# Kernel tuning notes

Measured on AMD Instinct MI355X. Metric: run time of the kernel, lower is better.

## Reference

```python
import jax, jax.numpy as jnp
import numpy as np

N = 50000
E = 800000


def sage_conv(x, edge_index, W_l, b_l, W_r):
    """PyG SAGEConv with mean aggregation.

    out = lin_l(mean_{j in N(i)} x_j) + lin_r(x_i)
    lin_l has bias, lin_r (root weight) has no bias.
    """
    src, dst = edge_index[0], edge_index[1]
    n = x.shape[0]
    msg_sum = jax.ops.segment_sum(x[src], dst, num_segments=n)          # [N, F]
    cnt = jax.ops.segment_sum(jnp.ones((edge_index.shape[1],), x.dtype), dst,
                              num_segments=n)                           # [N]
    mean = msg_sum / jnp.maximum(cnt, 1.0)[:, None]
    return mean @ W_l + b_l + x @ W_r


def setup_inputs() -> dict:
    key = jax.random.key(0)
    ks = jax.random.split(key, 10)
    dims = [(128, 128), (128, 128), (128, 64)]
    inp = {
        "x": jax.random.normal(ks[0], (N, 128), dtype=jnp.float32),
        "edge_index": jax.random.randint(ks[1], (2, E), 0, N, dtype=jnp.int64),
    }
    for i, (fi, fo) in enumerate(dims):
        scale = 1.0 / np.sqrt(fi)
        inp[f"W_l{i}"] = jax.random.uniform(ks[2 + 3 * i - (3 * i) % 1], (fi, fo), jnp.float32, -scale, scale)
        inp[f"b_l{i}"] = jnp.zeros((fo,), jnp.float32)
        inp[f"W_r{i}"] = jax.random.uniform(jax.random.fold_in(ks[3], i), (fi, fo), jnp.float32, -scale, scale)
        inp[f"W_l{i}"] = jax.random.uniform(jax.random.fold_in(ks[2], i), (fi, fo), jnp.float32, -scale, scale)
    return inp


def reference(x, edge_index, W_l0, b_l0, W_r0, W_l1, b_l1, W_r1, W_l2, b_l2, W_r2):
    # Layer 1 + relu (dropout identity in eval mode)
    h = jax.nn.relu(sage_conv(x, edge_index, W_l0, b_l0, W_r0))
    # Layer 2 + relu
    h = jax.nn.relu(sage_conv(h, edge_index, W_l1, b_l1, W_r1))
    # Output layer (no activation)
    return sage_conv(h, edge_index, W_l2, b_l2, W_r2)
```

## Files before the change

### kernel.cpp

```cpp
#include <hip/hip_runtime.h>

static inline int ceil_div(int a, int b) { return (a + b - 1) / b; }

typedef __attribute__((ext_vector_type(8))) short short8;
typedef __attribute__((ext_vector_type(4))) float f32x4;

__device__ __forceinline__ ushort bf16_rne(float v) {
  uint u = __float_as_uint(v);
  return (ushort)((u + 0x7FFFu + ((u >> 16) & 1u)) >> 16);
}


__global__ void k_zero_int(int* __restrict__ p, int n) {
  int i = blockIdx.x * blockDim.x + threadIdx.x;
  if (i < n) p[i] = 0;
}

__global__ void k_count_rank(const int* __restrict__ dst, int* __restrict__ cnt,
                             int* __restrict__ rank, int e) {
  int i0 = (blockIdx.x * blockDim.x + threadIdx.x) * 4;
  if (i0 >= e) return;
  int d[4], r[4];
  if (i0 + 3 < e) {
    int4 dv = *(const int4*)(dst + i0);
    d[0] = dv.x; d[1] = dv.y; d[2] = dv.z; d[3] = dv.w;
  } else {
#pragma unroll
    for (int j = 0; j < 4; ++j) d[j] = (i0 + j < e) ? dst[i0 + j] : 0;
  }
#pragma unroll
  for (int j = 0; j < 4; ++j)
    if (i0 + j < e) r[j] = atomicAdd(&cnt[d[j]], 1);
  if (i0 + 3 < e) {
    *(int4*)(rank + i0) = make_int4(r[0], r[1], r[2], r[3]);
  } else {
#pragma unroll
    for (int j = 0; j < 4; ++j)
      if (i0 + j < e) rank[i0 + j] = r[j];
  }
}

#define SCAN_BS 256
#define SCAN_VPT 4
#define SCAN_CHUNK (SCAN_BS * SCAN_VPT)

__global__ __launch_bounds__(SCAN_BS) void k_blocksum(const int* __restrict__ cnt,
                                                      int* __restrict__ partial, int n) {
  __shared__ int s[SCAN_BS / 64];
  const int tid = threadIdx.x;
  const int base = blockIdx.x * SCAN_CHUNK;
  int sum = 0;
#pragma unroll
  for (int j = 0; j < SCAN_VPT; ++j) {
    int i = base + tid + j * SCAN_BS;
    if (i < n) sum += cnt[i];
  }
#pragma unroll
  for (int off = 32; off > 0; off >>= 1) sum += __shfl_down(sum, off, 64);
  if ((tid & 63) == 0) s[tid >> 6] = sum;
  __syncthreads();
  if (tid == 0) {
    int t = 0;
#pragma unroll
    for (int w = 0; w < SCAN_BS / 64; ++w) t += s[w];
    partial[blockIdx.x] = t;
  }
}

__global__ __launch_bounds__(256) void k_scan_partials(int* __restrict__ partial, int p,
                                                       int* __restrict__ row_ptr, int n_nodes) {
  __shared__ int s[256];
  const int tid = threadIdx.x;
  int carry = 0;
  for (int base = 0; base < p; base += 256) {
    int i = base + tid;
    int v = (i < p) ? partial[i] : 0;
    s[tid] = v;
    __syncthreads();
    for (int off = 1; off < 256; off <<= 1) {
      int t = (tid >= off) ? s[tid - off] : 0;
      __syncthreads();
      s[tid] += t;
      __syncthreads();
    }
    if (i < p) partial[i] = carry + s[tid] - v;
    int tot = s[255];
    __syncthreads();
    carry += tot;
  }
  if (tid == 0) row_ptr[n_nodes] = carry;
}

__global__ __launch_bounds__(SCAN_BS) void k_scatter(const int* __restrict__ cnt,
                                                     const int* __restrict__ partial,
                                                     int* __restrict__ row_ptr,
                                                     float* __restrict__ inv, int n) {
  __shared__ int s[SCAN_BS];
  const int tid = threadIdx.x;
  const int base = blockIdx.x * SCAN_CHUNK;
  const int i0 = base + tid * SCAN_VPT;
  int v[SCAN_VPT];
  int cv[SCAN_VPT];
  int sum = 0;
#pragma unroll
  for (int j = 0; j < SCAN_VPT; ++j) {
    int i = i0 + j;
    int c = (i < n) ? cnt[i] : 0;
    cv[j] = c;
    v[j] = sum;
    sum += c;
  }
  s[tid] = sum;
  __syncthreads();
  for (int off = 1; off < SCAN_BS; off <<= 1) {
    int t = (tid >= off) ? s[tid - off] : 0;
    __syncthreads();
    s[tid] += t;
    __syncthreads();
  }
  const int excl = partial[blockIdx.x] + s[tid] - sum;
#pragma unroll
  for (int j = 0; j < SCAN_VPT; ++j) {
    int i = i0 + j;
    if (i < n) {
      row_ptr[i] = excl + v[j];
      inv[i] = 1.0f / (float)(cv[j] > 1 ? cv[j] : 1);
    }
  }
}

__global__ void k_place(const int* __restrict__ src, const int* __restrict__ dst,
                        const int* __restrict__ rank, const int* __restrict__ row_ptr,
                        ushort* __restrict__ csr16, int e) {
  int i0 = (blockIdx.x * blockDim.x + threadIdx.x) * 4;
  if (i0 >= e) return;
  if (i0 + 3 < e) {
    int4 dv = *(const int4*)(dst + i0);
    int4 sv = *(const int4*)(src + i0);
    int4 rv = *(const int4*)(rank + i0);
    int p0 = row_ptr[dv.x], p1 = row_ptr[dv.y], p2 = row_ptr[dv.z], p3 = row_ptr[dv.w];
    csr16[p0 + rv.x] = (ushort)sv.x;
    csr16[p1 + rv.y] = (ushort)sv.y;
    csr16[p2 + rv.z] = (ushort)sv.z;
    csr16[p3 + rv.w] = (ushort)sv.w;
  } else {
#pragma unroll
    for (int j = 0; j < 4; ++j) {
      int i = i0 + j;
      if (i < e) csr16[row_ptr[dst[i]] + rank[i]] = (ushort)src[i];
    }
  }
}

template <int FOUT>
__global__ void k_pack(const float* __restrict__ Wl, const float* __restrict__ Wr,
                       ushort* __restrict__ hi, ushort* __restrict__ lo) {
  constexpr int NCOL = 2 * FOUT;
  constexpr int NCHUNK = 4 * NCOL * 4;
  int ct = blockIdx.x * 256 + threadIdx.x;
  if (ct >= NCHUNK) return;
  const int g = ct & 3;
  const int nn = (ct >> 2) % NCOL;
  const int kt = ct / (4 * NCOL);
  uint hw[4], lw[4];
#pragma unroll
  for (int w = 0; w < 4; ++w) {
    uint h2[2], l2[2];
#pragma unroll
    for (int t = 0; t < 2; ++t) {
      int j = 2 * w + t;
      int k = kt * 32 + g * 8 + j;
      float v = (nn < FOUT) ? Wl[k * FOUT + nn] : Wr[k * FOUT + (nn - FOUT)];
      uint u = __float_as_uint(v);
      uint h = u >> 16;
      float r = v - __uint_as_float(h << 16);
      uint l = __float_as_uint(r) >> 16;
      h2[t] = h; l2[t] = l;
    }
    hw[w] = h2[0] | (h2[1] << 16);
    lw[w] = l2[0] | (l2[1] << 16);
  }
  ((uint4*)hi)[ct] = make_uint4(hw[0], hw[1], hw[2], hw[3]);
  ((uint4*)lo)[ct] = make_uint4(lw[0], lw[1], lw[2], lw[3]);
}

template <int FOUT>
__global__ __launch_bounds__(256) void k_gemm2(const float* __restrict__ hin,
                                               const ushort* __restrict__ Whi,
                                               const ushort* __restrict__ Wlo,
                                               const float* __restrict__ bias,
                                               ushort* __restrict__ Zb,
                                               float* __restrict__ R, int n) {
  constexpr int NCOL = 2 * FOUT;
  constexpr int NT = NCOL / 64;
  constexpr int MT = 2;
  __shared__ uint4 sA[2][32 * 16];

  const int tid = threadIdx.x;
  const int lane = tid & 63;
  const int wave = tid >> 6;
  const int row0 = blockIdx.x * 32;

  {
    const int srow = tid >> 3;
    const int kc = tid & 7;
    float4 f4[4];
    int g = row0 + srow;
    if (g < n) {
      const float4* hp = (const float4*)(hin + (size_t)g * 128 + kc * 16);
      f4[0] = hp[0]; f4[1] = hp[1]; f4[2] = hp[2]; f4[3] = hp[3];
    } else {
      f4[0] = f4[1] = f4[2] = f4[3] = make_float4(0.f, 0.f, 0.f, 0.f);
    }
    const float* fp = (const float*)f4;
#pragma unroll
    for (int b = 0; b < 2; ++b) {
      uint hw[4], lw[4];
#pragma unroll
      for (int w = 0; w < 4; ++w) {
        float a0 = fp[b * 8 + 2 * w], a1 = fp[b * 8 + 2 * w + 1];
        uint u0 = __float_as_uint(a0), u1 = __float_as_uint(a1);
        uint h0 = u0 >> 16, h1 = u1 >> 16;
        float r0 = a0 - __uint_as_float(h0 << 16);
        float r1 = a1 - __uint_as_float(h1 << 16);
        uint l0 = __float_as_uint(r0) >> 16, l1 = __float_as_uint(r1) >> 16;
        hw[w] = h0 | (h1 << 16);
        lw[w] = l0 | (l1 << 16);
      }
      int slot = (kc * 2 + b) ^ (srow & 7);
      sA[0][srow * 16 + slot] = make_uint4(hw[0], hw[1], hw[2], hw[3]);
      sA[1][srow * 16 + slot] = make_uint4(lw[0], lw[1], lw[2], lw[3]);
    }
  }
  __syncthreads();

  const int n0 = wave * (NCOL / 4);
  const int g16 = lane >> 4;
  const int l16 = lane & 15;

  f32x4 acc[MT][NT];
#pragma unroll
  for (int mt = 0; mt < MT; ++mt)
#pragma unroll
    for (int nt = 0; nt < NT; ++nt) acc[mt][nt] = (f32x4)(0.f);

#pragma unroll
  for (int kt = 0; kt < 4; ++kt) {
    short8 ahi[MT], alo[MT];
#pragma unroll
    for (int mt = 0; mt < MT; ++mt) {
      int row = mt * 16 + l16;
      int slot = (kt * 4 + g16) ^ (row & 7);
      ahi[mt] = *(const short8*)&sA[0][row * 16 + slot];
      alo[mt] = *(const short8*)&sA[1][row * 16 + slot];
    }
    short8 bh[NT];
#pragma unroll
    for (int nt = 0; nt < NT; ++nt) {
      size_t chunk = (size_t)(kt * NCOL + n0 + nt * 16 + l16) * 4 + g16;
      bh[nt] = *(const short8*)(Whi + chunk * 8);
    }
#pragma unroll
    for (int mt = 0; mt < MT; ++mt)
#pragma unroll
      for (int nt = 0; nt < NT; ++nt)
        acc[mt][nt] = __builtin_amdgcn_mfma_f32_16x16x32_bf16(ahi[mt], bh[nt], acc[mt][nt], 0, 0, 0);
#pragma unroll
    for (int mt = 0; mt < MT; ++mt)
#pragma unroll
      for (int nt = 0; nt < NT; ++nt)
        acc[mt][nt] = __builtin_amdgcn_mfma_f32_16x16x32_bf16(alo[mt], bh[nt], acc[mt][nt], 0, 0, 0);
    short8 bl[NT];
#pragma unroll
    for (int nt = 0; nt < NT; ++nt) {
      size_t chunk = (size_t)(kt * NCOL + n0 + nt * 16 + l16) * 4 + g16;
      bl[nt] = *(const short8*)(Wlo + chunk * 8);
    }
#pragma unroll
    for (int mt = 0; mt < MT; ++mt)
#pragma unroll
      for (int nt = 0; nt < NT; ++nt)
        acc[mt][nt] = __builtin_amdgcn_mfma_f32_16x16x32_bf16(ahi[mt], bl[nt], acc[mt][nt], 0, 0, 0);
  }

#pragma unroll
  for (int nt = 0; nt < NT; ++nt) {
    int col = n0 + nt * 16 + l16;
    bool isR = col >= FOUT;
    int cw = isR ? col - FOUT : col;
    float badd = isR ? bias[cw] : 0.f;
#pragma unroll
    for (int mt = 0; mt < MT; ++mt) {
#pragma unroll
      for (int j = 0; j < 4; ++j) {
        int row = row0 + mt * 16 + g16 * 4 + j;
        if (row < n) {
          float v = acc[mt][nt][j] + badd;
          if (isR) R[(size_t)row * FOUT + cw] = v;
          else Zb[(size_t)row * FOUT + cw] = bf16_rne(v);
        }
      }
    }
  }
}

template <int FOUT>
__global__ __launch_bounds__(256) void k_gemm2b(const ushort* __restrict__ Hb,
                                                const ushort* __restrict__ Whi,
                                                const ushort* __restrict__ Wlo,
                                                const float* __restrict__ bias,
                                                ushort* __restrict__ Zb,
                                                float* __restrict__ R, int n) {
  constexpr int NCOL = 2 * FOUT;
  constexpr int NT = NCOL / 64;
  constexpr int MT = 2;
  __shared__ uint4 sA[32 * 16];

  const int tid = threadIdx.x;
  const int lane = tid & 63;
  const int wave = tid >> 6;
  const int row0 = blockIdx.x * 32;

#pragma unroll
  for (int c = tid; c < 512; c += 256) {
    int srow = c >> 4, col16 = c & 15;
    int g = row0 + srow;
    uint4 v = make_uint4(0u, 0u, 0u, 0u);
    if (g < n) v = *(const uint4*)(Hb + (size_t)g * 128 + col16 * 8);
    sA[srow * 16 + (col16 ^ (srow & 7))] = v;
  }
  __syncthreads();

  const int n0 = wave * (NCOL / 4);
  const int g16 = lane >> 4;
  const int l16 = lane & 15;

  f32x4 acc[MT][NT];
#pragma unroll
  for (int mt = 0; mt < MT; ++mt)
#pragma unroll
    for (int nt = 0; nt < NT; ++nt) acc[mt][nt] = (f32x4)(0.f);

#pragma unroll
  for (int kt = 0; kt < 4; ++kt) {
    short8 a[MT];
#pragma unroll
    for (int mt = 0; mt < MT; ++mt) {
      int row = mt * 16 + l16;
      int slot = (kt * 4 + g16) ^ (row & 7);
      a[mt] = *(const short8*)&sA[row * 16 + slot];
    }
    short8 bh[NT], bl[NT];
#pragma unroll
    for (int nt = 0; nt < NT; ++nt) {
      size_t chunk = (size_t)(kt * NCOL + n0 + nt * 16 + l16) * 4 + g16;
      bh[nt] = *(const short8*)(Whi + chunk * 8);
      bl[nt] = *(const short8*)(Wlo + chunk * 8);
    }
#pragma unroll
    for (int mt = 0; mt < MT; ++mt)
#pragma unroll
      for (int nt = 0; nt < NT; ++nt)
        acc[mt][nt] = __builtin_amdgcn_mfma_f32_16x16x32_bf16(a[mt], bh[nt], acc[mt][nt], 0, 0, 0);
#pragma unroll
    for (int mt = 0; mt < MT; ++mt)
#pragma unroll
      for (int nt = 0; nt < NT; ++nt)
        acc[mt][nt] = __builtin_amdgcn_mfma_f32_16x16x32_bf16(a[mt], bl[nt], acc[mt][nt], 0, 0, 0);
  }

#pragma unroll
  for (int nt = 0; nt < NT; ++nt) {
    int col = n0 + nt * 16 + l16;
    bool isR = col >= FOUT;
    int cw = isR ? col - FOUT : col;
    float badd = isR ? bias[cw] : 0.f;
#pragma unroll
    for (int mt = 0; mt < MT; ++mt) {
#pragma unroll
      for (int j = 0; j < 4; ++j) {
        int row = row0 + mt * 16 + g16 * 4 + j;
        if (row < n) {
          float v = acc[mt][nt][j] + badd;
          if (isR) R[(size_t)row * FOUT + cw] = v;
          else Zb[(size_t)row * FOUT + cw] = bf16_rne(v);
        }
      }
    }
  }
}

template <int FOUT, bool RELU, bool OUTB>
__global__ __launch_bounds__(256) void k_agg2(const ushort* __restrict__ Zb,
                                              const float* __restrict__ R,
                                              const int* __restrict__ row_ptr,
                                              const ushort* __restrict__ csr16,
                                              const float* __restrict__ inv,
                                              void* __restrict__ outp, int n) {
  constexpr int FL = FOUT / 8;
  constexpr int EG = 64 / FL;
  const int lane = threadIdx.x & 63;
  const int node = blockIdx.x * 4 + (threadIdx.x >> 6);
  if (node >= n) return;
  const int c = lane % FL;
  const int eg = lane / FL;

  const int e0 = row_ptr[node];
  const int m = row_ptr[node + 1] - e0;
  const uint4* Z4 = (const uint4*)Zb;

  float acc[8];
#pragma unroll
  for (int k = 0; k < 8; ++k) acc[k] = 0.f;

  int t = eg;
  while (t < m) {
    int ss[4];
#pragma unroll
    for (int j = 0; j < 4; ++j) {
      int tj = t + j * EG;
      int tc = (tj < m) ? tj : (m - 1);
      ss[j] = csr16[e0 + tc];
    }
    uint4 z[4];
#pragma unroll
    for (int j = 0; j < 4; ++j) z[j] = Z4[(size_t)ss[j] * FL + c];
#pragma unroll
    for (int j = 0; j < 4; ++j) {
      if (t + j * EG < m) {
        const uint* zw = (const uint*)&z[j];
#pragma unroll
        for (int w = 0; w < 4; ++w) {
          acc[2 * w]     += __uint_as_float(zw[w] << 16);
          acc[2 * w + 1] += __uint_as_float(zw[w] & 0xFFFF0000u);
        }
      }
    }
    t += 4 * EG;
  }

#pragma unroll
  for (int off = FL; off < 64; off <<= 1) {
#pragma unroll
    for (int k = 0; k < 8; ++k) acc[k] += __shfl_xor(acc[k], off, 64);
  }

  if (eg == 0) {
    const float iv = inv[node];
    const float4* Rp = (const float4*)(R + (size_t)node * FOUT + c * 8);
    float4 r0 = Rp[0], r1 = Rp[1];
    float o[8];
    o[0] = fmaf(acc[0], iv, r0.x);
    o[1] = fmaf(acc[1], iv, r0.y);
    o[2] = fmaf(acc[2], iv, r0.z);
    o[3] = fmaf(acc[3], iv, r0.w);
    o[4] = fmaf(acc[4], iv, r1.x);
    o[5] = fmaf(acc[5], iv, r1.y);
    o[6] = fmaf(acc[6], iv, r1.z);
    o[7] = fmaf(acc[7], iv, r1.w);
    if (RELU) {
#pragma unroll
      for (int k = 0; k < 8; ++k) o[k] = fmaxf(o[k], 0.f);
    }
    if (OUTB) {
      uint p[4];
#pragma unroll
      for (int w = 0; w < 4; ++w)
        p[w] = (uint)bf16_rne(o[2 * w]) | ((uint)bf16_rne(o[2 * w + 1]) << 16);
      ((uint4*)outp)[(size_t)node * FL + c] = make_uint4(p[0], p[1], p[2], p[3]);
    } else {
      float4* op = (float4*)((float*)outp + (size_t)node * FOUT + c * 8);
      op[0] = make_float4(o[0], o[1], o[2], o[3]);
      op[1] = make_float4(o[4], o[5], o[6], o[7]);
    }
  }
}


extern "C" void kernel_launch(void* const* d_in, const int* in_sizes, int n_in,
                              void* d_out, int out_size, void* d_ws, size_t ws_size,
                              hipStream_t stream) {
  const float* x   = (const float*)d_in[0];
  const int*   ei  = (const int*)d_in[1];
  const float* Wl0 = (const float*)d_in[2];
  const float* bl0 = (const float*)d_in[3];
  const float* Wr0 = (const float*)d_in[4];
  const float* Wl1 = (const float*)d_in[5];
  const float* bl1 = (const float*)d_in[6];
  const float* Wr1 = (const float*)d_in[7];
  const float* Wl2 = (const float*)d_in[8];
  const float* bl2 = (const float*)d_in[9];
  const float* Wr2 = (const float*)d_in[10];
  float* out = (float*)d_out;

  const int N = in_sizes[0] / 128;
  const int E = in_sizes[1] / 2;
  const int* src = ei;
  const int* dst = ei + E;

  char* w = (char*)d_ws;
  auto alloc = [&](size_t bytes) {
    char* p = w;
    w += (bytes + 255) & ~(size_t)255;
    return p;
  };
  int*    cnt     = (int*)alloc((size_t)N * 4);
  int*    row_ptr = (int*)alloc((size_t)(N + 1) * 4);
  int*    rank    = (int*)alloc((size_t)E * 4);
  ushort* csr16   = (ushort*)alloc((size_t)E * 2 + 256);
  float*  inv     = (float*)alloc((size_t)N * 4);
  int*    partial = (int*)alloc((size_t)ceil_div(N, SCAN_CHUNK) * 4 + 256);
  ushort* Whi0    = (ushort*)alloc((size_t)4 * 256 * 4 * 16);
  ushort* Wlo0    = (ushort*)alloc((size_t)4 * 256 * 4 * 16);
  ushort* Whi1    = (ushort*)alloc((size_t)4 * 256 * 4 * 16);
  ushort* Wlo1    = (ushort*)alloc((size_t)4 * 256 * 4 * 16);
  ushort* Whi2    = (ushort*)alloc((size_t)4 * 128 * 4 * 16);
  ushort* Wlo2    = (ushort*)alloc((size_t)4 * 128 * 4 * 16);
  ushort* BZ      = (ushort*)alloc((size_t)N * 128 * 2);
  float*  BR      = (float*)alloc((size_t)N * 128 * 4);
  ushort* B0      = (ushort*)alloc((size_t)N * 128 * 2);
  (void)ws_size; (void)n_in; (void)out_size;

  const int P = ceil_div(N, SCAN_CHUNK);

  k_pack<128><<<16, 256, 0, stream>>>(Wl0, Wr0, Whi0, Wlo0);
  k_pack<128><<<16, 256, 0, stream>>>(Wl1, Wr1, Whi1, Wlo1);
  k_pack<64><<<8, 256, 0, stream>>>(Wl2, Wr2, Whi2, Wlo2);

  k_zero_int<<<ceil_div(N, 256), 256, 0, stream>>>(cnt, N);
  k_count_rank<<<ceil_div(E, 1024), 256, 0, stream>>>(dst, cnt, rank, E);
  k_blocksum<<<P, SCAN_BS, 0, stream>>>(cnt, partial, N);
  k_scan_partials<<<1, 256, 0, stream>>>(partial, P, row_ptr, N);
  k_scatter<<<P, SCAN_BS, 0, stream>>>(cnt, partial, row_ptr, inv, N);
  k_place<<<ceil_div(E, 1024), 256, 0, stream>>>(src, dst, rank, row_ptr, csr16, E);

  k_gemm2<128><<<ceil_div(N, 32), 256, 0, stream>>>(x, Whi0, Wlo0, bl0, BZ, BR, N);
  k_agg2<128, true, true><<<ceil_div(N, 4), 256, 0, stream>>>(BZ, BR, row_ptr, csr16, inv, B0, N);

  k_gemm2b<128><<<ceil_div(N, 32), 256, 0, stream>>>(B0, Whi1, Wlo1, bl1, BZ, BR, N);
  k_agg2<128, true, true><<<ceil_div(N, 4), 256, 0, stream>>>(BZ, BR, row_ptr, csr16, inv, B0, N);

  k_gemm2b<64><<<ceil_div(N, 32), 256, 0, stream>>>(B0, Whi2, Wlo2, bl2, BZ, BR, N);
  k_agg2<64, false, false><<<ceil_div(N, 4), 256, 0, stream>>>(BZ, BR, row_ptr, csr16, inv, out, N);
}
```

Measured before the change: 232.4 us.

## Fuse edge count into first GEMM launch and double GEMM row tile

Merges the degree-count/rank kernel into the first-layer GEMM as extra blocks of one launch, so the atomic counting runs alongside the dense transform instead of in a separate launch. It also raises the GEMM row tile from 32 to 64 rows per block (MT 2→4) in all three GEMMs, reusing loaded weight fragments across more rows. The trade-off is more registers and LDS per block, which may lower occupancy, and a heterogeneous grid mixing two kinds of work.

```diff
diff --git a/kernel.cpp b/kernel.cpp
--- a/kernel.cpp
+++ b/kernel.cpp
@@ -14,30 +14,6 @@
 __global__ void k_zero_int(int* __restrict__ p, int n) {
   int i = blockIdx.x * blockDim.x + threadIdx.x;
   if (i < n) p[i] = 0;
-}
-
-__global__ void k_count_rank(const int* __restrict__ dst, int* __restrict__ cnt,
-                             int* __restrict__ rank, int e) {
-  int i0 = (blockIdx.x * blockDim.x + threadIdx.x) * 4;
-  if (i0 >= e) return;
-  int d[4], r[4];
-  if (i0 + 3 < e) {
-    int4 dv = *(const int4*)(dst + i0);
-    d[0] = dv.x; d[1] = dv.y; d[2] = dv.z; d[3] = dv.w;
-  } else {
-#pragma unroll
-    for (int j = 0; j < 4; ++j) d[j] = (i0 + j < e) ? dst[i0 + j] : 0;
-  }
-#pragma unroll
-  for (int j = 0; j < 4; ++j)
-    if (i0 + j < e) r[j] = atomicAdd(&cnt[d[j]], 1);
-  if (i0 + 3 < e) {
-    *(int4*)(rank + i0) = make_int4(r[0], r[1], r[2], r[3]);
-  } else {
-#pragma unroll
-    for (int j = 0; j < 4; ++j)
-      if (i0 + j < e) rank[i0 + j] = r[j];
-  }
 }
 
 #define SCAN_BS 256
@@ -184,37 +160,63 @@
   ((uint4*)lo)[ct] = make_uint4(lw[0], lw[1], lw[2], lw[3]);
 }
 
-template <int FOUT>
-__global__ __launch_bounds__(256) void k_gemm2(const float* __restrict__ hin,
-                                               const ushort* __restrict__ Whi,
-                                               const ushort* __restrict__ Wlo,
-                                               const float* __restrict__ bias,
-                                               ushort* __restrict__ Zb,
-                                               float* __restrict__ R, int n) {
+__global__ __launch_bounds__(256) void k_gemm0_count(
+    const float* __restrict__ hin, const ushort* __restrict__ Whi,
+    const ushort* __restrict__ Wlo, const float* __restrict__ bias,
+    ushort* __restrict__ Zb, float* __restrict__ R, int n, int gemmBlocks,
+    const int* __restrict__ dstv, int* __restrict__ cnt, int* __restrict__ rank, int e) {
+  constexpr int FOUT = 128;
   constexpr int NCOL = 2 * FOUT;
   constexpr int NT = NCOL / 64;
-  constexpr int MT = 2;
-  __shared__ uint4 sA[2][32 * 16];
+  constexpr int MT = 4;
+  __shared__ uint4 sA[2][64 * 16];
 
   const int tid = threadIdx.x;
+
+  if (blockIdx.x >= gemmBlocks) {
+    int i0 = ((blockIdx.x - gemmBlocks) * 256 + tid) * 4;
+    if (i0 >= e) return;
+    int d[4], r[4];
+    if (i0 + 3 < e) {
+      int4 dv = *(const int4*)(dstv + i0);
+      d[0] = dv.x; d[1] = dv.y; d[2] = dv.z; d[3] = dv.w;
+    } else {
+#pragma unroll
+      for (int j = 0; j < 4; ++j) d[j] = (i0 + j < e) ? dstv[i0 + j] : 0;
+    }
+#pragma unroll
+    for (int j = 0; j < 4; ++j)
+      if (i0 + j < e) r[j] = atomicAdd(&cnt[d[j]], 1);
+    if (i0 + 3 < e) {
+      *(int4*)(rank + i0) = make_int4(r[0], r[1], r[2], r[3]);
+    } else {
+#pragma unroll
+      for (int j = 0; j < 4; ++j)
+        if (i0 + j < e) rank[i0 + j] = r[j];
+    }
+    return;
+  }
+
   const int lane = tid & 63;
   const int wave = tid >> 6;
-  const int row0 = blockIdx.x * 32;
+  const int row0 = blockIdx.x * 64;
 
   {
-    const int srow = tid >> 3;
-    const int kc = tid & 7;
-    float4 f4[4];
+    const int srow = tid >> 2;
+    const int kc = tid & 3;
+    float4 f4[8];
     int g = row0 + srow;
     if (g < n) {
-      const float4* hp = (const float4*)(hin + (size_t)g * 128 + kc * 16);
-      f4[0] = hp[0]; f4[1] = hp[1]; f4[2] = hp[2]; f4[3] = hp[3];
+      const float4* hp = (const float4*)(hin + (size_t)g * 128 + kc * 32);
+#pragma unroll
+      for (int w = 0; w < 8; ++w) f4[w] = hp[w];
     } else {
-      f4[0] = f4[1] = f4[2] = f4[3] = make_float4(0.f, 0.f, 0.f, 0.f);
+#pragma unroll
+      for (int w = 0; w < 8; ++w) f4[w] = make_float4(0.f, 0.f, 0.f, 0.f);
     }
     const float* fp = (const float*)f4;
 #pragma unroll
-    for (int b = 0; b < 2; ++b) {
+    for (int b = 0; b < 4; ++b) {
       uint hw[4], lw[4];
 #pragma unroll
       for (int w = 0; w < 4; ++w) {
@@ -227,7 +229,7 @@
         hw[w] = h0 | (h1 << 16);
         lw[w] = l0 | (l1 << 16);
       }
-      int slot = (kc * 2 + b) ^ (srow & 7);
+      int slot = (kc * 4 + b) ^ (srow & 7);
       sA[0][srow * 16 + slot] = make_uint4(hw[0], hw[1], hw[2], hw[3]);
       sA[1][srow * 16 + slot] = make_uint4(lw[0], lw[1], lw[2], lw[3]);
     }
@@ -313,16 +315,16 @@
                                                 float* __restrict__ R, int n) {
   constexpr int NCOL = 2 * FOUT;
   constexpr int NT = NCOL / 64;
-  constexpr int MT = 2;
-  __shared__ uint4 sA[32 * 16];
+  constexpr int MT = 4;
+  __shared__ uint4 sA[64 * 16];
 
   const int tid = threadIdx.x;
   const int lane = tid & 63;
   const int wave = tid >> 6;
-  const int row0 = blockIdx.x * 32;
-
-#pragma unroll
-  for (int c = tid; c < 512; c += 256) {
+  const int row0 = blockIdx.x * 64;
+
+#pragma unroll
+  for (int c = tid; c < 1024; c += 256) {
     int srow = c >> 4, col16 = c & 15;
     int g = row0 + srow;
     uint4 v = make_uint4(0u, 0u, 0u, 0u);
@@ -522,24 +524,27 @@
   (void)ws_size; (void)n_in; (void)out_size;
 
   const int P = ceil_div(N, SCAN_CHUNK);
+  const int G0 = ceil_div(N, 64);
+  const int C0 = ceil_div(E, 1024);
 
   k_pack<128><<<16, 256, 0, stream>>>(Wl0, Wr0, Whi0, Wlo0);
   k_pack<128><<<16, 256, 0, stream>>>(Wl1, Wr1, Whi1, Wlo1);
   k_pack<64><<<8, 256, 0, stream>>>(Wl2, Wr2, Whi2, Wlo2);
 
   k_zero_int<<<ceil_div(N, 256), 256, 0, stream>>>(cnt, N);
-  k_count_rank<<<ceil_div(E, 1024), 256, 0, stream>>>(dst, cnt, rank, E);
+  k_gemm0_count<<<G0 + C0, 256, 0, stream>>>(x, Whi0, Wlo0, bl0, BZ, BR, N, G0,
+                                             dst, cnt, rank, E);
+
   k_blocksum<<<P, SCAN_BS, 0, stream>>>(cnt, partial, N);
   k_scan_partials<<<1, 256, 0, stream>>>(partial, P, row_ptr, N);
   k_scatter<<<P, SCAN_BS, 0, stream>>>(cnt, partial, row_ptr, inv, N);
   k_place<<<ceil_div(E, 1024), 256, 0, stream>>>(src, dst, rank, row_ptr, csr16, E);
 
-  k_gemm2<128><<<ceil_div(N, 32), 256, 0, stream>>>(x, Whi0, Wlo0, bl0, BZ, BR, N);
   k_agg2<128, true, true><<<ceil_div(N, 4), 256, 0, stream>>>(BZ, BR, row_ptr, csr16, inv, B0, N);
 
-  k_gemm2b<128><<<ceil_div(N, 32), 256, 0, stream>>>(B0, Whi1, Wlo1, bl1, BZ, BR, N);
+  k_gemm2b<128><<<ceil_div(N, 64), 256, 0, stream>>>(B0, Whi1, Wlo1, bl1, BZ, BR, N);
   k_agg2<128, true, true><<<ceil_div(N, 4), 256, 0, stream>>>(BZ, BR, row_ptr, csr16, inv, B0, N);
 
-  k_gemm2b<64><<<ceil_div(N, 32), 256, 0, stream>>>(B0, Whi2, Wlo2, bl2, BZ, BR, N);
+  k_gemm2b<64><<<ceil_div(N, 64), 256, 0, stream>>>(B0, Whi2, Wlo2, bl2, BZ, BR, N);
   k_agg2<64, false, false><<<ceil_div(N, 4), 256, 0, stream>>>(BZ, BR, row_ptr, csr16, inv, out, N);
 }
```

After: 240.8 us. +3.6%, slower.
